# Performance work log

Measured on AMD Instinct MI355X. Metric: run time of the kernel, lower is better.

The kernel has to match this reference:

```python
import jax, jax.numpy as jnp
import numpy as np

D_MODEL = 1024
N_HEADS = 16
D_K = D_MODEL // N_HEADS
MIN_F = 3
MAX_F = 10


def setup_inputs() -> dict:
    key = jax.random.key(0)
    ks = jax.random.split(key, 9)
    B, L = 4, 8192
    x = jax.random.normal(ks[0], (B, L, D_MODEL), jnp.float32)
    def w(k):
        return jax.random.normal(k, (D_MODEL, D_MODEL), jnp.float32) * 0.02
    def b(k):
        return jax.random.normal(k, (D_MODEL,), jnp.float32) * 0.02
    return {
        'x': x,
        'wq': w(ks[1]), 'bq': b(ks[2]),
        'wk': w(ks[3]), 'bk': b(ks[4]),
        'wv': w(ks[5]), 'bv': b(ks[6]),
        'wo': w(ks[7]), 'bo': b(ks[8]),
    }


def _sparsity_score(Q):
    # Q: (B, H, L, d_k)
    l2 = jnp.linalg.norm(Q, axis=-1)
    logp = jax.nn.log_softmax(Q, axis=-1)
    prob = jnp.exp(logp)
    entropy = -jnp.sum(prob * jnp.log(prob + 1e-9), axis=-1)
    var = jnp.var(Q, axis=-1, ddof=1)  # torch.var is unbiased by default
    return 0.5 * l2 + 0.3 * entropy + 0.2 * var


def reference(x, wq, bq, wk, bk, wv, bv, wo, bo):
    B, L, D = x.shape
    H, dk = N_HEADS, D_K
    # torch Linear: y = x @ W.T + b
    Q = (x @ wq.T + bq).reshape(B, L, H, dk).transpose(0, 2, 1, 3)  # (B,H,L,dk)
    K = (x @ wk.T + bk).reshape(B, L, H, dk).transpose(0, 2, 1, 3)
    V = (x @ wv.T + bv).reshape(B, L, H, dk).transpose(0, 2, 1, 3)

    q_scores = _sparsity_score(Q)  # (B,H,L)
    q_std = jnp.std(q_scores, axis=2, keepdims=True, ddof=1)
    q_mean = jnp.mean(q_scores, axis=2, keepdims=True)
    factor = jnp.clip(
        jnp.round(q_std / (q_mean + 1e-6) * MAX_F).astype(jnp.int32),
        MIN_F, MAX_F)  # (B,H,1)
    u = factor[:, 0, 0]  # per-batch k, taken from head 0 (matches torch code)

    # Fixed-size top-k of MAX_F; rows beyond u are masked to zero.
    _, top_idx = jax.lax.top_k(q_scores, MAX_F)  # (B,H,MAX_F)
    mask = (jnp.arange(MAX_F)[None, None, :] < u[:, None, None])  # (B,1->H,MAX_F)

    Q_sparse = jnp.take_along_axis(Q, top_idx[..., None], axis=2)  # (B,H,MAX_F,dk)
    scores = jnp.einsum('bhud,bhld->bhul', Q_sparse, K) / np.sqrt(dk).astype(np.float32)
    attn = jax.nn.softmax(scores, axis=-1)
    out = jnp.einsum('bhul,bhld->bhud', attn, V)  # (B,H,MAX_F,dk)
    out = out * mask[..., None].astype(out.dtype)

    # Scatter back into zeros; top-k indices are distinct per (b,h), so writing
    # masked zeros at the extra indices leaves those rows zero as in torch.
    bi = jnp.arange(B)[:, None, None]
    hi = jnp.arange(H)[None, :, None]
    full = jnp.zeros((B, H, L, dk), out.dtype).at[bi, hi, top_idx].set(out)

    merged = full.transpose(0, 2, 1, 3).reshape(B, L, D)
    return merged @ wo.T + bo
```

## Files before the change

kernel.cpp:

```cpp
#include <hip/hip_runtime.h>
#include <cmath>


typedef short     s16x8 __attribute__((ext_vector_type(8)));
typedef unsigned short u16x8 __attribute__((ext_vector_type(8)));
typedef unsigned short u16x4 __attribute__((ext_vector_type(4)));
typedef float     f32x4 __attribute__((ext_vector_type(4)));

__device__ __forceinline__ unsigned short f2bf(float f) {
    unsigned u = __float_as_uint(f);
    u += 0x7fffu + ((u >> 16) & 1u);
    return (unsigned short)(u >> 16);
}
__device__ __forceinline__ float bf2f(unsigned short s) {
    return __uint_as_float(((unsigned)s) << 16);
}

__device__ __forceinline__ void async16(const void* g, void* l) {
    __builtin_amdgcn_global_load_lds(
        (const __attribute__((address_space(1))) void*)g,
        (__attribute__((address_space(3))) void*)l, 16, 0, 0);
}

__global__ void k_conv(const float* __restrict__ x, const float* __restrict__ wq,
                       const float* __restrict__ wk, const float* __restrict__ wv,
                       unsigned short* __restrict__ xb, unsigned short* __restrict__ wb) {
    size_t i = (size_t)blockIdx.x * 256 + threadIdx.x;
    if (i < 8388608) {
        float4 v = ((const float4*)x)[i];
        ushort4 o; o.x = f2bf(v.x); o.y = f2bf(v.y); o.z = f2bf(v.z); o.w = f2bf(v.w);
        ((ushort4*)xb)[i] = o;
    } else {
        size_t j = i - 8388608;
        size_t wsel = j >> 18, rem = j & 262143;
        const float* src = wsel == 0 ? wq : (wsel == 1 ? wk : wv);
        float4 v = ((const float4*)src)[rem];
        ushort4 o; o.x = f2bf(v.x); o.y = f2bf(v.y); o.z = f2bf(v.z); o.w = f2bf(v.w);
        ((ushort4*)wb)[j] = o;
    }
}

__global__ __launch_bounds__(512, 2) void k_gemm_qkv(
    const unsigned short* __restrict__ xb, const unsigned short* __restrict__ wb,
    const float* __restrict__ bq, const float* __restrict__ bk, const float* __restrict__ bv,
    unsigned short* __restrict__ Kb, unsigned short* __restrict__ Vb,
    float* __restrict__ scores)
{
    extern __shared__ char ldsb[];
    int bid = blockIdx.x;
    int mt = bid / 12, ntile = bid % 12;
    int wsel = ntile >> 2, ntq = ntile & 3;
    int tid = threadIdx.x, wid = tid >> 6, lane = tid & 63;
    int wm = wid >> 2, wn = wid & 3;
    int ml = lane & 15, quad = lane >> 4;

    const char* xg = (const char*)(xb + (size_t)mt * 256 * 1024);
    const char* wg = (const char*)(wb + (size_t)ntile * 256 * 1024);

    int rg0  = wid * 2;
    int rsub = lane >> 3;
    int cswz = ((lane & 7) ^ rsub) << 4;

#define STAGE(gbase_, roff_) do {                                          \
        const char* _g = (gbase_) + (size_t)(rg0 * 8 + rsub) * 2048 + cswz; \
        char* _l = ldsb + (roff_) + rg0 * 1024;                             \
        async16(_g, _l);                                                    \
        async16(_g + 8 * 2048, _l + 1024);                                  \
    } while (0)

    int q0  = (quad * 16) ^ ((ml & 7) << 4);
    int qk0 = q0, qk1 = q0 ^ 64;
    int aconst = wm * 16384 + ml * 128;
    int bconst = 32768 + (wn >> 1) * 16384 + (wn & 1) * 8192 + ml * 128;

    f32x4 acc[8][4] = {};

    STAGE(wg,                32768);
    STAGE(wg + 262144,       32768 + 16384);
    STAGE(xg,                0);
    STAGE(xg + 262144,       16384);
    STAGE(wg + 128,          65536 + 32768);
    STAGE(wg + 262144 + 128, 65536 + 32768 + 16384);
    asm volatile("s_waitcnt vmcnt(4)" ::: "memory");
    __builtin_amdgcn_s_barrier();
    asm volatile("" ::: "memory");

    for (int t = 0; t < 16; ++t) {
        int buf  = (t & 1) << 16;
        int nbuf = buf ^ 65536;
        const char* A_ = ldsb + buf + aconst;
        const char* B_ = ldsb + buf + bconst;
        s16x8 bfr[4][2];
#pragma unroll
        for (int p = 0; p < 4; ++p) {
            if (p == 0) {
#pragma unroll
                for (int n = 0; n < 4; ++n) {
                    bfr[n][0] = *(const s16x8*)(B_ + n * 2048 + qk0);
                    bfr[n][1] = *(const s16x8*)(B_ + n * 2048 + qk1);
                }
            }
            s16x8 am0[2], am1[2];
            am0[0] = *(const s16x8*)(A_ + (2 * p) * 2048 + qk0);
            am0[1] = *(const s16x8*)(A_ + (2 * p) * 2048 + qk1);
            am1[0] = *(const s16x8*)(A_ + (2 * p + 1) * 2048 + qk0);
            am1[1] = *(const s16x8*)(A_ + (2 * p + 1) * 2048 + qk1);
            if (p == 0 && t < 15) STAGE(xg + (size_t)(t + 1) * 128, nbuf);
            if (p == 1 && t < 15) STAGE(xg + 262144 + (size_t)(t + 1) * 128, nbuf + 16384);
            if (p == 2 && t < 14) STAGE(wg + (size_t)(t + 2) * 128, buf + 32768);
            if (p == 3 && t < 14) STAGE(wg + 262144 + (size_t)(t + 2) * 128, buf + 32768 + 16384);
            asm volatile("" ::: "memory");
            __builtin_amdgcn_s_barrier();
            asm volatile("" ::: "memory");
            __builtin_amdgcn_s_setprio(1);
#pragma unroll
            for (int kk = 0; kk < 2; ++kk)
#pragma unroll
                for (int n = 0; n < 4; ++n) {
                    acc[2 * p][n]     = __builtin_amdgcn_mfma_f32_16x16x32_bf16(am0[kk], bfr[n][kk], acc[2 * p][n], 0, 0, 0);
                    acc[2 * p + 1][n] = __builtin_amdgcn_mfma_f32_16x16x32_bf16(am1[kk], bfr[n][kk], acc[2 * p + 1][n], 0, 0, 0);
                }
            __builtin_amdgcn_s_setprio(0);
            if (p == 3) {
                if (t <= 13)      asm volatile("s_waitcnt vmcnt(4)" ::: "memory");
                else if (t == 14) asm volatile("s_waitcnt vmcnt(0)" ::: "memory");
            }
            asm volatile("" ::: "memory");
            __builtin_amdgcn_s_barrier();
            asm volatile("" ::: "memory");
        }
    }
#undef STAGE

    float bvv[4];
    const float* bias = wsel == 0 ? bq : (wsel == 1 ? bk : bv);
    int colbase = ntq * 256 + wn * 64;
#pragma unroll
    for (int n = 0; n < 4; ++n) bvv[n] = bias[colbase + n * 16 + ml];

    if (wsel == 0) {
        int hh = ntq * 4 + wn;
#pragma unroll
        for (int m = 0; m < 8; ++m) {
#pragma unroll
            for (int r = 0; r < 4; ++r) {
                float q0v = acc[m][0][r] + bvv[0];
                float q1v = acc[m][1][r] + bvv[1];
                float q2v = acc[m][2][r] + bvv[2];
                float q3v = acc[m][3][r] + bvv[3];
                float mx = fmaxf(fmaxf(q0v, q1v), fmaxf(q2v, q3v));
                float sm = q0v + q1v + q2v + q3v;
                float ss = q0v * q0v + q1v * q1v + q2v * q2v + q3v * q3v;
#pragma unroll
                for (int off = 1; off < 16; off <<= 1) {
                    mx = fmaxf(mx, __shfl_xor(mx, off));
                    sm += __shfl_xor(sm, off);
                    ss += __shfl_xor(ss, off);
                }
                float e0 = expf(q0v - mx), e1 = expf(q1v - mx);
                float e2 = expf(q2v - mx), e3 = expf(q3v - mx);
                float S = e0 + e1 + e2 + e3;
#pragma unroll
                for (int off = 1; off < 16; off <<= 1) S += __shfl_xor(S, off);
                float is = 1.f / S;
                float p0 = e0 * is, p1 = e1 * is, p2 = e2 * is, p3 = e3 * is;
                float ent = -p0 * logf(p0 + 1e-9f) - p1 * logf(p1 + 1e-9f)
                            - p2 * logf(p2 + 1e-9f) - p3 * logf(p3 + 1e-9f);
                float mean = sm * (1.f / 64.f);
                float d0 = q0v - mean, d1 = q1v - mean, d2 = q2v - mean, d3 = q3v - mean;
                float var = d0 * d0 + d1 * d1 + d2 * d2 + d3 * d3;
#pragma unroll
                for (int off = 1; off < 16; off <<= 1) {
                    ent += __shfl_xor(ent, off);
                    var += __shfl_xor(var, off);
                }
                if (ml == 0) {
                    float sc = 0.5f * sqrtf(ss) + 0.3f * ent + 0.2f * (var * (1.f / 63.f));
                    int row = mt * 256 + wm * 128 + m * 16 + quad * 4 + r;
                    scores[(size_t)(((row >> 13) << 4) + hh) * 8192 + (row & 8191)] = sc;
                }
            }
        }
    } else {
        unsigned short* outp = wsel == 1 ? Kb : Vb;
#pragma unroll
        for (int m = 0; m < 8; ++m) {
            int grow0 = mt * 256 + wm * 128 + m * 16 + quad * 4;
#pragma unroll
            for (int n = 0; n < 4; ++n) {
                int gcol = colbase + n * 16 + ml;
#pragma unroll
                for (int r = 0; r < 4; ++r)
                    outp[(size_t)(grow0 + r) * 1024 + gcol] = f2bf(acc[m][n][r] + bvv[n]);
            }
        }
    }
}

__global__ __launch_bounds__(1024) void k_cand(const float* __restrict__ scores,
                                               int* __restrict__ cand, int* __restrict__ u)
{
    int pair = blockIdx.x; int t = threadIdx.x;
    __shared__ float  s_lds[8192];
    __shared__ double dred[1024];
    __shared__ float  wvv[16];
    __shared__ int    wii[16];
    const float* sp = scores + (size_t)pair * 8192;
    for (int i = t; i < 8192; i += 1024) s_lds[i] = sp[i];
    __syncthreads();

    if ((pair & 15) == 0) {
        double a0 = 0;
#pragma unroll
        for (int k = 0; k < 8; ++k) a0 += (double)s_lds[t + k * 1024];
        dred[t] = a0; __syncthreads();
        for (int st = 512; st > 0; st >>= 1) { if (t < st) dred[t] += dred[t + st]; __syncthreads(); }
        double mean = dred[0] / 8192.0;
        __syncthreads();
        double a1 = 0;
#pragma unroll
        for (int k = 0; k < 8; ++k) { double d = (double)s_lds[t + k * 1024] - mean; a1 += d * d; }
        dred[t] = a1; __syncthreads();
        for (int st = 512; st > 0; st >>= 1) { if (t < st) dred[t] += dred[t + st]; __syncthreads(); }
        if (t == 0) {
            double sd = sqrt(dred[0] / 8191.0);
            double ratio = sd / (mean + 1e-6) * 10.0;
            int f = (int)rint(ratio);
            f = f < 3 ? 3 : (f > 10 ? 10 : f);
            u[pair >> 4] = f;
        }
        __syncthreads();
    }

    for (int it = 0; it < 16; ++it) {
        float bv = -1e30f; int bi = 0x7fffffff;
#pragma unroll
        for (int k = 0; k < 8; ++k) {
            int i = t + k * 1024;
            float v = s_lds[i];
            if (v > bv || (v == bv && i < bi)) { bv = v; bi = i; }
        }
#pragma unroll
        for (int off = 32; off > 0; off >>= 1) {
            float ov = __shfl_down(bv, off);
            int   oi = __shfl_down(bi, off);
            if (ov > bv || (ov == bv && oi < bi)) { bv = ov; bi = oi; }
        }
        if ((t & 63) == 0) { wvv[t >> 6] = bv; wii[t >> 6] = bi; }
        __syncthreads();
        if (t == 0) {
            float fv = wvv[0]; int fi = wii[0];
            for (int k = 1; k < 16; ++k)
                if (wvv[k] > fv || (wvv[k] == fv && wii[k] < fi)) { fv = wvv[k]; fi = wii[k]; }
            cand[pair * 16 + it] = fi;
            s_lds[fi] = -1e30f;
        }
        __syncthreads();
    }
}

__global__ __launch_bounds__(256) void k_rescore(
    const int* __restrict__ cand, const float* __restrict__ x,
    const float* __restrict__ wq, const float* __restrict__ bq,
    double* __restrict__ cscore, float* __restrict__ cq)
{
    int bid = blockIdx.x;
    int pair = bid >> 4;
    int b = pair >> 4, h = pair & 15;
    int t = threadIdx.x;
    __shared__ float  xrow[1024];
    __shared__ double dred[256];
    __shared__ double qrow[64];

    int l = cand[bid];
    const float* xr = x + ((size_t)b * 8192 + l) * 1024;
    for (int i = t; i < 1024; i += 256) xrow[i] = xr[i];
    __syncthreads();

    int d = t >> 2, ks = t & 3;
    const float* wr = wq + (size_t)(h * 64 + d) * 1024 + ks * 256;
    const float* xs = xrow + ks * 256;
    double p = 0;
    for (int k = 0; k < 256; k += 4) {
        float4 w4 = *(const float4*)(wr + k);
        float4 x4 = *(const float4*)(xs + k);
        p += (double)w4.x * x4.x + (double)w4.y * x4.y +
             (double)w4.z * x4.z + (double)w4.w * x4.w;
    }
    dred[t] = p; __syncthreads();
    if ((t & 3) == 0)
        qrow[t >> 2] = dred[t] + dred[t + 1] + dred[t + 2] + dred[t + 3] + (double)bq[h * 64 + (t >> 2)];
    __syncthreads();

    if (t < 64) {
        double q = qrow[t];
        cq[(size_t)bid * 64 + t] = (float)q;
        double m = q;
#pragma unroll
        for (int off = 32; off > 0; off >>= 1) m = fmax(m, __shfl_down(m, off));
        m = __shfl(m, 0);
        double e = exp(q - m);
        double sum = q, sumsq = q * q, S = e;
#pragma unroll
        for (int off = 32; off > 0; off >>= 1) {
            sum += __shfl_down(sum, off);
            sumsq += __shfl_down(sumsq, off);
            S += __shfl_down(S, off);
        }
        sum = __shfl(sum, 0); sumsq = __shfl(sumsq, 0); S = __shfl(S, 0);
        double pp = e / S;
        double entc = -pp * log(pp + 1e-9);
        double mean = sum / 64.0;
        double dv = q - mean;
        double varc = dv * dv;
#pragma unroll
        for (int off = 32; off > 0; off >>= 1) {
            entc += __shfl_down(entc, off);
            varc += __shfl_down(varc, off);
        }
        if (t == 0)
            cscore[bid] = 0.5 * sqrt(sumsq) + 0.3 * entc + 0.2 * (varc / 63.0);
    }
}

__global__ void k_select(const int* __restrict__ cand, const double* __restrict__ cscore,
                         const float* __restrict__ cq,
                         int* __restrict__ sel, float* __restrict__ selq)
{
    int pair = blockIdx.x; int t = threadIdx.x;
    __shared__ int order[10];
    if (t == 0) {
        bool used[16] = {};
        for (int r = 0; r < 10; ++r) {
            int best = -1;
            for (int c = 0; c < 16; ++c) {
                if (used[c]) continue;
                int ic = pair * 16 + c;
                if (best < 0 || cscore[ic] > cscore[pair * 16 + best] ||
                    (cscore[ic] == cscore[pair * 16 + best] && cand[ic] < cand[pair * 16 + best]))
                    best = c;
            }
            used[best] = true; order[r] = best;
            sel[pair * 10 + r] = cand[pair * 16 + best];
        }
    }
    __syncthreads();
    for (int r = 0; r < 10; ++r)
        selq[((size_t)pair * 10 + r) * 64 + t] = cq[((size_t)pair * 16 + order[r]) * 64 + t];
}

__global__ __launch_bounds__(256) void k_attn_part(
    const unsigned short* __restrict__ Kb, const unsigned short* __restrict__ Vb,
    const float* __restrict__ selq, const int* __restrict__ u,
    float* __restrict__ part)
{
    int bid = blockIdx.x;
    int pair = bid >> 5, chunk = bid & 31;
    int b = pair >> 4, h = pair & 15;
    int uu = u[b];
    int t = threadIdx.x, wave = t >> 6, lane = t & 63;

    __shared__ float q_sh[10][64];
    __shared__ float w_sh[10][256];
    __shared__ unsigned short V_sh[256][68];
    __shared__ float mc_sh[10][2], Sc_sh[10][2];

    size_t kvbase = ((size_t)b * 8192 + (size_t)chunk * 256) * 1024 + h * 64;

    for (int i = t; i < uu * 64; i += 256)
        q_sh[i >> 6][i & 63] = selq[(size_t)pair * 640 + i] * 0.125f;

    const u16x8* kr = (const u16x8*)(Kb + kvbase + (size_t)t * 1024);
    const u16x8* vr = (const u16x8*)(Vb + kvbase + (size_t)t * 1024);
    u16x8 vreg[8];
#pragma unroll
    for (int k8 = 0; k8 < 8; ++k8) vreg[k8] = vr[k8];
#pragma unroll
    for (int k8 = 0; k8 < 8; ++k8) {
        *(u16x4*)&V_sh[t][k8 * 8]     = { vreg[k8][0], vreg[k8][1], vreg[k8][2], vreg[k8][3] };
        *(u16x4*)&V_sh[t][k8 * 8 + 4] = { vreg[k8][4], vreg[k8][5], vreg[k8][6], vreg[k8][7] };
    }
    float krow[64];
#pragma unroll
    for (int k8 = 0; k8 < 8; ++k8) {
        u16x8 kv = kr[k8];
#pragma unroll
        for (int e = 0; e < 8; ++e) krow[k8 * 8 + e] = bf2f(kv[e]);
    }
    __syncthreads();

    for (int rr = 0; rr < uu; ++rr) {
        const float4* qp = (const float4*)q_sh[rr];
        float acc = 0.f;
#pragma unroll
        for (int i4 = 0; i4 < 16; ++i4) {
            float4 q4 = qp[i4];
            acc += q4.x * krow[i4 * 4] + q4.y * krow[i4 * 4 + 1] +
                   q4.z * krow[i4 * 4 + 2] + q4.w * krow[i4 * 4 + 3];
        }
        w_sh[rr][t] = acc;
    }
    __syncthreads();

    for (int rr = wave; rr < uu; rr += 4) {
        float4 wv = *(const float4*)&w_sh[rr][lane * 4];
        float m4 = fmaxf(fmaxf(wv.x, wv.y), fmaxf(wv.z, wv.w));
#pragma unroll
        for (int off = 16; off > 0; off >>= 1) m4 = fmaxf(m4, __shfl_xor(m4, off));
        float e0 = expf(wv.x - m4), e1 = expf(wv.y - m4);
        float e2 = expf(wv.z - m4), e3 = expf(wv.w - m4);
        float s = e0 + e1 + e2 + e3;
#pragma unroll
        for (int off = 16; off > 0; off >>= 1) s += __shfl_xor(s, off);
        float4 ev = { e0, e1, e2, e3 };
        *(float4*)&w_sh[rr][lane * 4] = ev;
        if ((lane & 31) == 0) { int jh = lane >> 5; mc_sh[rr][jh] = m4; Sc_sh[rr][jh] = s; }
    }
    __syncthreads();

    int jh = t >> 7, tt = t & 127, dp = tt & 31;
    for (int rr = tt >> 5; rr < uu; rr += 4) {
        float o0 = 0.f, o1 = 0.f;
        int j0 = jh * 128;
        for (int j = j0; j < j0 + 128; j += 4) {
            float4 w4 = *(const float4*)&w_sh[rr][j];
#pragma unroll
            for (int jj = 0; jj < 4; ++jj) {
                unsigned v = *(const unsigned*)&V_sh[j + jj][dp * 2];
                float w1 = jj == 0 ? w4.x : (jj == 1 ? w4.y : (jj == 2 ? w4.z : w4.w));
                o0 += w1 * __uint_as_float(v << 16);
                o1 += w1 * __uint_as_float(v & 0xffff0000u);
            }
        }
        float* pp = part + (((size_t)pair * 10 + rr) * 64 + chunk * 2 + jh) * 66;
        float2 o2 = { o0, o1 };
        *(float2*)&pp[2 + dp * 2] = o2;
        if (dp == 0) { pp[0] = mc_sh[rr][jh]; pp[1] = Sc_sh[rr][jh]; }
    }
}

__global__ void k_bias(const float* __restrict__ bo, float* __restrict__ out) {
    size_t i = (size_t)blockIdx.x * 256 + threadIdx.x;
    int col4 = (int)(i & 255);
    ((float4*)out)[i] = ((const float4*)bo)[col4];
}

__global__ __launch_bounds__(256) void k_mergescatter(
    const float* __restrict__ part, const int* __restrict__ sel,
    const int* __restrict__ u, const float* __restrict__ wo,
    float* __restrict__ out)
{
    int idx = blockIdx.x; int pair = idx / 10; int r = idx % 10;
    int b = pair >> 4, h = pair & 15;
    if (r >= u[b]) return;
    int t = threadIdx.x;
    __shared__ float a_sh[64];
    if (t < 64) {
        const float* base = part + ((size_t)pair * 10 + r) * 64 * 66;
        float m = -1e30f;
        for (int c = 0; c < 64; ++c) m = fmaxf(m, base[c * 66]);
        float S = 0, o = 0;
        for (int c = 0; c < 64; ++c) {
            float f = expf(base[c * 66] - m);
            S += f * base[c * 66 + 1];
            o += f * base[c * 66 + 2 + t];
        }
        a_sh[t] = o / S;
    }
    __syncthreads();
    int l = sel[pair * 10 + r];
    float* orow = out + ((size_t)b * 8192 + l) * 1024;
    for (int j = t; j < 1024; j += 256) {
        const float* wr = wo + (size_t)j * 1024 + h * 64;
        float acc = 0;
#pragma unroll
        for (int d = 0; d < 64; d += 4) {
            float4 w4 = *(const float4*)(wr + d);
            acc += a_sh[d] * w4.x + a_sh[d + 1] * w4.y + a_sh[d + 2] * w4.z + a_sh[d + 3] * w4.w;
        }
        atomicAdd(orow + j, acc);
    }
}

static constexpr size_t OFF_XB    = 0;
static constexpr size_t OFF_WB    = OFF_XB + 67108864;
static constexpr size_t OFF_KB    = OFF_WB + 6291456;
static constexpr size_t OFF_VB    = OFF_KB + 67108864;
static constexpr size_t OFF_SC    = OFF_VB + 67108864;
static constexpr size_t OFF_U     = OFF_SC + 2097152;
static constexpr size_t OFF_SEL   = OFF_U + 256;
static constexpr size_t OFF_SELQ  = OFF_SEL + 4096;
static constexpr size_t OFF_PART  = OFF_SELQ + 163840;
static constexpr size_t OFF_CAND  = OFF_PART + 10813440;
static constexpr size_t OFF_CSC   = OFF_CAND + 4096;
static constexpr size_t OFF_CQ    = OFF_CSC + 8192;
static constexpr size_t WS_NEED   = OFF_CQ + 262144;

extern "C" void kernel_launch(void* const* d_in, const int* in_sizes, int n_in,
                              void* d_out, int out_size, void* d_ws, size_t ws_size,
                              hipStream_t stream)
{
    const float* x  = (const float*)d_in[0];
    const float* wq = (const float*)d_in[1];
    const float* bq = (const float*)d_in[2];
    const float* wk = (const float*)d_in[3];
    const float* bk = (const float*)d_in[4];
    const float* wv = (const float*)d_in[5];
    const float* bv = (const float*)d_in[6];
    const float* wo = (const float*)d_in[7];
    const float* bo = (const float*)d_in[8];
    float* out = (float*)d_out;

    if (ws_size < WS_NEED) return;

    char* ws = (char*)d_ws;
    unsigned short* xb = (unsigned short*)(ws + OFF_XB);
    unsigned short* wb = (unsigned short*)(ws + OFF_WB);
    unsigned short* Kb = (unsigned short*)(ws + OFF_KB);
    unsigned short* Vb = (unsigned short*)(ws + OFF_VB);
    float*  scores = (float*)(ws + OFF_SC);
    int*    u      = (int*)(ws + OFF_U);
    int*    sel    = (int*)(ws + OFF_SEL);
    float*  selq   = (float*)(ws + OFF_SELQ);
    float*  part   = (float*)(ws + OFF_PART);
    int*    cand   = (int*)(ws + OFF_CAND);
    double* cscore = (double*)(ws + OFF_CSC);
    float*  cq     = (float*)(ws + OFF_CQ);

    k_conv        <<<35840, 256,  0,      stream>>>(x, wq, wk, wv, xb, wb);
    k_gemm_qkv    <<<1536,  512,  131072, stream>>>(xb, wb, bq, bk, bv, Kb, Vb, scores);
    k_cand        <<<64,    1024, 0,      stream>>>(scores, cand, u);
    k_rescore     <<<1024,  256,  0,      stream>>>(cand, x, wq, bq, cscore, cq);
    k_select      <<<64,    64,   0,      stream>>>(cand, cscore, cq, sel, selq);
    k_attn_part   <<<2048,  256,  0,      stream>>>(Kb, Vb, selq, u, part);
    k_bias        <<<32768, 256,  0,      stream>>>(bo, out);
    k_mergescatter<<<640,   256,  0,      stream>>>(part, sel, u, wo, out);
}
```

Before: 759.9 us.

## Cut QKV GEMM barriers per k-step and double-buffer A fragment reads

The QKV GEMM inner loop used to run four sub-phases per k-step, each with two workgroup barriers. It now reads all B fragments once and ping-pongs A fragments between two register sets, so each LDS read overlaps the MFMAs of the previous pair. Only two barriers remain per k-step, and the global-to-LDS staging calls are interleaved between the MFMA groups. This removes most barrier stalls but needs more live registers, and it depends on the barrier placement still guarding the LDS buffer reuse.

```diff
diff --git a/kernel.cpp b/kernel.cpp
--- a/kernel.cpp
+++ b/kernel.cpp
@@ -40,6 +40,26 @@
     }
 }
 
+__device__ __forceinline__ void rdA(s16x8 (&dst)[2][2], const char* A_, int r0,
+                                    int qk0, int qk1) {
+    dst[0][0] = *(const s16x8*)(A_ + r0 * 2048 + qk0);
+    dst[0][1] = *(const s16x8*)(A_ + r0 * 2048 + qk1);
+    dst[1][0] = *(const s16x8*)(A_ + (r0 + 1) * 2048 + qk0);
+    dst[1][1] = *(const s16x8*)(A_ + (r0 + 1) * 2048 + qk1);
+}
+__device__ __forceinline__ void mfma8(f32x4 (&acc)[8][4], int i0, int i1,
+                                      const s16x8 (&aa)[2][2], const s16x8 (&bfr)[4][2]) {
+    __builtin_amdgcn_s_setprio(1);
+#pragma unroll
+    for (int kk = 0; kk < 2; ++kk)
+#pragma unroll
+        for (int n = 0; n < 4; ++n) {
+            acc[i0][n] = __builtin_amdgcn_mfma_f32_16x16x32_bf16(aa[0][kk], bfr[n][kk], acc[i0][n], 0, 0, 0);
+            acc[i1][n] = __builtin_amdgcn_mfma_f32_16x16x32_bf16(aa[1][kk], bfr[n][kk], acc[i1][n], 0, 0, 0);
+        }
+    __builtin_amdgcn_s_setprio(0);
+}
+
 __global__ __launch_bounds__(512, 2) void k_gemm_qkv(
     const unsigned short* __restrict__ xb, const unsigned short* __restrict__ wb,
     const float* __restrict__ bq, const float* __restrict__ bk, const float* __restrict__ bv,
@@ -92,43 +112,31 @@
         const char* B_ = ldsb + buf + bconst;
         s16x8 bfr[4][2];
 #pragma unroll
-        for (int p = 0; p < 4; ++p) {
-            if (p == 0) {
-#pragma unroll
-                for (int n = 0; n < 4; ++n) {
-                    bfr[n][0] = *(const s16x8*)(B_ + n * 2048 + qk0);
-                    bfr[n][1] = *(const s16x8*)(B_ + n * 2048 + qk1);
-                }
-            }
-            s16x8 am0[2], am1[2];
-            am0[0] = *(const s16x8*)(A_ + (2 * p) * 2048 + qk0);
-            am0[1] = *(const s16x8*)(A_ + (2 * p) * 2048 + qk1);
-            am1[0] = *(const s16x8*)(A_ + (2 * p + 1) * 2048 + qk0);
-            am1[1] = *(const s16x8*)(A_ + (2 * p + 1) * 2048 + qk1);
-            if (p == 0 && t < 15) STAGE(xg + (size_t)(t + 1) * 128, nbuf);
-            if (p == 1 && t < 15) STAGE(xg + 262144 + (size_t)(t + 1) * 128, nbuf + 16384);
-            if (p == 2 && t < 14) STAGE(wg + (size_t)(t + 2) * 128, buf + 32768);
-            if (p == 3 && t < 14) STAGE(wg + 262144 + (size_t)(t + 2) * 128, buf + 32768 + 16384);
-            asm volatile("" ::: "memory");
-            __builtin_amdgcn_s_barrier();
-            asm volatile("" ::: "memory");
-            __builtin_amdgcn_s_setprio(1);
-#pragma unroll
-            for (int kk = 0; kk < 2; ++kk)
-#pragma unroll
-                for (int n = 0; n < 4; ++n) {
-                    acc[2 * p][n]     = __builtin_amdgcn_mfma_f32_16x16x32_bf16(am0[kk], bfr[n][kk], acc[2 * p][n], 0, 0, 0);
-                    acc[2 * p + 1][n] = __builtin_amdgcn_mfma_f32_16x16x32_bf16(am1[kk], bfr[n][kk], acc[2 * p + 1][n], 0, 0, 0);
-                }
-            __builtin_amdgcn_s_setprio(0);
-            if (p == 3) {
-                if (t <= 13)      asm volatile("s_waitcnt vmcnt(4)" ::: "memory");
-                else if (t == 14) asm volatile("s_waitcnt vmcnt(0)" ::: "memory");
-            }
-            asm volatile("" ::: "memory");
-            __builtin_amdgcn_s_barrier();
-            asm volatile("" ::: "memory");
-        }
+        for (int n = 0; n < 4; ++n) {
+            bfr[n][0] = *(const s16x8*)(B_ + n * 2048 + qk0);
+            bfr[n][1] = *(const s16x8*)(B_ + n * 2048 + qk1);
+        }
+        s16x8 af[2][2], ag[2][2];
+        rdA(af, A_, 0, qk0, qk1);
+        if (t < 15) STAGE(xg + (size_t)(t + 1) * 128, nbuf);
+        rdA(ag, A_, 2, qk0, qk1);
+        mfma8(acc, 0, 1, af, bfr);
+        if (t < 15) STAGE(xg + 262144 + (size_t)(t + 1) * 128, nbuf + 16384);
+        rdA(af, A_, 4, qk0, qk1);
+        mfma8(acc, 2, 3, ag, bfr);
+        asm volatile("" ::: "memory");
+        __builtin_amdgcn_s_barrier();
+        asm volatile("" ::: "memory");
+        if (t < 14) STAGE(wg + (size_t)(t + 2) * 128, buf + 32768);
+        rdA(ag, A_, 6, qk0, qk1);
+        mfma8(acc, 4, 5, af, bfr);
+        if (t < 14) STAGE(wg + 262144 + (size_t)(t + 2) * 128, buf + 32768 + 16384);
+        mfma8(acc, 6, 7, ag, bfr);
+        if (t <= 13)      asm volatile("s_waitcnt vmcnt(4)" ::: "memory");
+        else if (t == 14) asm volatile("s_waitcnt vmcnt(0)" ::: "memory");
+        asm volatile("" ::: "memory");
+        __builtin_amdgcn_s_barrier();
+        asm volatile("" ::: "memory");
     }
 #undef STAGE
 
```

After: 710.3 us. 6.5% less time.
